# Kernel optimization log

Hardware: AMD Instinct MI355X
Metric: run time of the kernel (lower is better)

## Reference

```python
import jax, jax.numpy as jnp
import numpy as np

N_NODES = 50000
N_EDGES = 800000
NFEAT = 64
HID = 64
NCLASS = 10


def setup_inputs() -> dict:
    key = jax.random.key(0)
    ks = jax.random.split(key, 12)
    x = jax.random.normal(ks[0], (N_NODES, NFEAT), dtype=jnp.float32)
    edge_index = jax.random.randint(ks[1], (2, N_EDGES), 0, N_NODES, dtype=jnp.int64)
    edge_attr = jax.random.uniform(ks[2], (N_EDGES,), dtype=jnp.float32)
    # GCNConv layer params (glorot-ish scale)
    W1 = jax.random.normal(ks[3], (NFEAT, HID), dtype=jnp.float32) / np.sqrt(NFEAT)
    b1 = jnp.zeros((HID,), dtype=jnp.float32)
    W2 = jax.random.normal(ks[4], (HID, HID), dtype=jnp.float32) / np.sqrt(HID)
    b2 = jnp.zeros((HID,), dtype=jnp.float32)
    fc1_w = jax.random.normal(ks[5], (HID, 128), dtype=jnp.float32) / np.sqrt(HID)
    fc1_b = jnp.zeros((128,), dtype=jnp.float32)
    fc2_w = jax.random.normal(ks[6], (128, NCLASS), dtype=jnp.float32) / np.sqrt(128.0)
    fc2_b = jnp.zeros((NCLASS,), dtype=jnp.float32)
    return {"x": x, "edge_index": edge_index, "edge_attr": edge_attr,
            "W1": W1, "b1": b1, "W2": W2, "b2": b2,
            "fc1_w": fc1_w, "fc1_b": fc1_b, "fc2_w": fc2_w, "fc2_b": fc2_b}


def reference(x, edge_index, edge_attr, W1, b1, W2, b2, fc1_w, fc1_b, fc2_w, fc2_b):
    N = x.shape[0]
    # add_self_loops: append (i, i) edges; self-loop edge weight = 1
    loops = jnp.arange(N, dtype=edge_index.dtype)
    row = jnp.concatenate([edge_index[0], loops])
    col = jnp.concatenate([edge_index[1], loops])
    ew = jnp.concatenate([edge_attr, jnp.ones((N,), dtype=x.dtype)])
    # symmetric degree normalization: deg = degree(row); D^{-1/2} A D^{-1/2}
    deg = jax.ops.segment_sum(jnp.ones_like(ew), row, num_segments=N)
    dis = deg ** -0.5  # deg >= 1 due to self loops
    norm_w = dis[row] * ew * dis[col]  # [E+N]

    def gcn_conv(h, W, b):
        h = h @ W                                    # [N, d_out]
        msg = norm_w[:, None] * h[col]               # [E+N, d_out] gather
        agg = jax.ops.segment_sum(msg, row, num_segments=N)  # scatter-add
        return agg + b

    h = jax.nn.relu(gcn_conv(x, W1, b1))  # dropout is identity in eval mode
    h = gcn_conv(h, W2, b2)               # no activation after last conv
    h = jax.nn.relu(h @ fc1_w + fc1_b)
    return h @ fc2_w + fc2_b
```

## Files before the change

kernel.cpp:

```cpp
#include <hip/hip_runtime.h>


#define NFEAT 64


__global__ void k_hist(const int* __restrict__ row, int* __restrict__ cnt, int ne) {
    int i = blockIdx.x * blockDim.x + threadIdx.x;
    int st = gridDim.x * blockDim.x;
    for (; i < ne; i += st) atomicAdd(&cnt[row[i]], 1);
}

__global__ void k_scanA(const int* __restrict__ cnt, int* __restrict__ bsum, int n) {
    __shared__ int s[256];
    int tid = threadIdx.x;
    int i = blockIdx.x * 256 + tid;
    s[tid] = (i < n) ? cnt[i] : 0;
    __syncthreads();
    for (int d = 128; d > 0; d >>= 1) {
        if (tid < d) s[tid] += s[tid + d];
        __syncthreads();
    }
    if (tid == 0) bsum[blockIdx.x] = s[0];
}

__global__ void k_scanB(const int* __restrict__ bsum, int* __restrict__ bpre, int nb) {
    __shared__ int s[256];
    int tid = threadIdx.x;
    int v = (tid < nb) ? bsum[tid] : 0;
    s[tid] = v;
    __syncthreads();
    for (int d = 1; d < 256; d <<= 1) {
        int t = (tid >= d) ? s[tid - d] : 0;
        __syncthreads();
        s[tid] += t;
        __syncthreads();
    }
    if (tid < nb) bpre[tid] = s[tid] - v;
}

__global__ void k_scanC(const int* __restrict__ cnt, const int* __restrict__ bpre,
                        int* __restrict__ off, float* __restrict__ dis, int n) {
    __shared__ int s[256];
    int tid = threadIdx.x;
    int i = blockIdx.x * 256 + tid;
    int v = (i < n) ? cnt[i] : 0;
    s[tid] = v;
    __syncthreads();
    for (int d = 1; d < 256; d <<= 1) {
        int t = (tid >= d) ? s[tid - d] : 0;
        __syncthreads();
        s[tid] += t;
        __syncthreads();
    }
    if (i < n) {
        off[i] = bpre[blockIdx.x] + s[tid] - v;
        dis[i] = rsqrtf(1.0f + (float)v);
    }
}

__global__ void k_fill(const int* __restrict__ row, const int* __restrict__ col,
                       const float* __restrict__ ew, const float* __restrict__ dis,
                       int* __restrict__ off, int2* __restrict__ csr, int ne) {
    int i = blockIdx.x * blockDim.x + threadIdx.x;
    if (i >= ne) return;
    int r = row[i], c = col[i];
    float w = dis[r] * ew[i] * dis[c];
    int slot = atomicAdd(&off[r], 1);
    csr[slot] = make_int2(c, __float_as_int(w));
}


__global__ __launch_bounds__(256) void k_gemm64(const float* __restrict__ X,
                                                const float* __restrict__ W,
                                                float* __restrict__ Y, int nrows) {
    __shared__ float Wl[64 * 64];
    __shared__ float XT[64 * 68];
    int tid = threadIdx.x;
    int r0 = blockIdx.x * 64;
    for (int i = tid; i < 64 * 64; i += 256) Wl[i] = W[i];
    for (int i = tid; i < 64 * 64; i += 256) {
        int r = i >> 6, k = i & 63;
        int rr = r0 + r;
        XT[k * 68 + r] = (rr < nrows) ? X[(size_t)r0 * 64 + i] : 0.f;
    }
    __syncthreads();
    int f4 = (tid & 15) * 4;
    int r4 = (tid >> 4) * 4;
    float acc[4][4];
#pragma unroll
    for (int i = 0; i < 4; ++i)
#pragma unroll
        for (int j = 0; j < 4; ++j) acc[i][j] = 0.f;
#pragma unroll 8
    for (int k = 0; k < 64; ++k) {
        float4 w = *(const float4*)&Wl[k * 64 + f4];
        float4 xv = *(const float4*)&XT[k * 68 + r4];
        float xs[4] = {xv.x, xv.y, xv.z, xv.w};
        float ws[4] = {w.x, w.y, w.z, w.w};
#pragma unroll
        for (int i = 0; i < 4; ++i)
#pragma unroll
            for (int j = 0; j < 4; ++j) acc[i][j] = fmaf(xs[i], ws[j], acc[i][j]);
    }
#pragma unroll
    for (int i = 0; i < 4; ++i) {
        int rr = r0 + r4 + i;
        if (rr < nrows) {
            float4 o = make_float4(acc[i][0], acc[i][1], acc[i][2], acc[i][3]);
            *(float4*)&Y[(size_t)rr * 64 + f4] = o;
        }
    }
}


__device__ __forceinline__ float4 agg_row(const int* off_end, const int* cnt,
                                          const int2* csr, const float* H,
                                          int node, int sub, int q4) {
    int endv = off_end[node];
    int s = endv - cnt[node];
    float4 acc = make_float4(0.f, 0.f, 0.f, 0.f);
    int e = s + sub;
    for (; e + 4 < endv; e += 8) {
        int2 p0 = csr[e];
        int2 p1 = csr[e + 4];
        float w0 = __int_as_float(p0.y);
        float w1 = __int_as_float(p1.y);
        float4 h0 = *(const float4*)&H[(size_t)p0.x * 64 + q4];
        float4 h1 = *(const float4*)&H[(size_t)p1.x * 64 + q4];
        acc.x = fmaf(w0, h0.x, acc.x);
        acc.y = fmaf(w0, h0.y, acc.y);
        acc.z = fmaf(w0, h0.z, acc.z);
        acc.w = fmaf(w0, h0.w, acc.w);
        acc.x = fmaf(w1, h1.x, acc.x);
        acc.y = fmaf(w1, h1.y, acc.y);
        acc.z = fmaf(w1, h1.z, acc.z);
        acc.w = fmaf(w1, h1.w, acc.w);
    }
    if (e < endv) {
        int2 p = csr[e];
        float w = __int_as_float(p.y);
        float4 h = *(const float4*)&H[(size_t)p.x * 64 + q4];
        acc.x = fmaf(w, h.x, acc.x);
        acc.y = fmaf(w, h.y, acc.y);
        acc.z = fmaf(w, h.z, acc.z);
        acc.w = fmaf(w, h.w, acc.w);
    }
#pragma unroll
    for (int m = 16; m <= 32; m <<= 1) {
        acc.x += __shfl_xor(acc.x, m, 64);
        acc.y += __shfl_xor(acc.y, m, 64);
        acc.z += __shfl_xor(acc.z, m, 64);
        acc.w += __shfl_xor(acc.w, m, 64);
    }
    return acc;
}


__global__ __launch_bounds__(256) void k_agg(const int* __restrict__ off_end,
                                             const int* __restrict__ cnt,
                                             const float* __restrict__ dis,
                                             const int2* __restrict__ csr,
                                             const float* __restrict__ H,
                                             float* __restrict__ AGG, int n) {
    int l = threadIdx.x & 63;
    int node = (blockIdx.x * blockDim.x + threadIdx.x) >> 6;
    if (node >= n) return;
    int sub = l >> 4;
    int q4 = (l & 15) * 4;
    float4 acc = agg_row(off_end, cnt, csr, H, node, sub, q4);
    if (sub == 0) {
        float d = dis[node];
        float d2 = d * d;
        float4 hs = *(const float4*)&H[(size_t)node * 64 + q4];
        acc.x = fmaf(d2, hs.x, acc.x);
        acc.y = fmaf(d2, hs.y, acc.y);
        acc.z = fmaf(d2, hs.z, acc.z);
        acc.w = fmaf(d2, hs.w, acc.w);
        *(float4*)&AGG[(size_t)node * 64 + q4] = acc;
    }
}


__global__ __launch_bounds__(256) void k_agg_fused(const int* __restrict__ off_end,
                                                   const int* __restrict__ cnt,
                                                   const float* __restrict__ dis,
                                                   const int2* __restrict__ csr,
                                                   const float* __restrict__ H1,
                                                   const float* __restrict__ b1,
                                                   const float* __restrict__ W2,
                                                   float* __restrict__ H2, int n) {
    __shared__ float W2l[64 * 64];
    __shared__ float pbuf[4][64];
    int tid = threadIdx.x;
    for (int i = tid; i < 64 * 64; i += 256) W2l[i] = W2[i];
    __syncthreads();
    int l = tid & 63;
    int wv = tid >> 6;
    int sub = l >> 4;
    int q4 = (l & 15) * 4;
    int nwaves = (gridDim.x * blockDim.x) >> 6;
    for (int node = (blockIdx.x * blockDim.x + tid) >> 6; node < n; node += nwaves) {
        float4 acc = agg_row(off_end, cnt, csr, H1, node, sub, q4);
        float d = dis[node];
        float d2 = d * d;
        float4 hs = *(const float4*)&H1[(size_t)node * 64 + q4];
        float4 bq = *(const float4*)&b1[q4];
        float4 p;
        p.x = fmaxf(fmaf(d2, hs.x, acc.x) + bq.x, 0.f);
        p.y = fmaxf(fmaf(d2, hs.y, acc.y) + bq.y, 0.f);
        p.z = fmaxf(fmaf(d2, hs.z, acc.z) + bq.z, 0.f);
        p.w = fmaxf(fmaf(d2, hs.w, acc.w) + bq.w, 0.f);
        if (sub == 0) *(float4*)&pbuf[wv][q4] = p;
        asm volatile("s_waitcnt lgkmcnt(0)" ::: "memory");
        float sum = 0.f;
#pragma unroll
        for (int q = 0; q < 16; ++q) {
            float4 v = *(const float4*)&pbuf[wv][q * 4];
            sum = fmaf(v.x, W2l[(q * 4 + 0) * 64 + l], sum);
            sum = fmaf(v.y, W2l[(q * 4 + 1) * 64 + l], sum);
            sum = fmaf(v.z, W2l[(q * 4 + 2) * 64 + l], sum);
            sum = fmaf(v.w, W2l[(q * 4 + 3) * 64 + l], sum);
        }
        asm volatile("s_waitcnt lgkmcnt(0)" ::: "memory");
        H2[(size_t)node * 64 + l] = sum;
    }
}


__global__ __launch_bounds__(256, 4) void k_mlp(const float* __restrict__ AGG,
                                                const float* __restrict__ b2,
                                                const float* __restrict__ fc1w,
                                                const float* __restrict__ fc1b,
                                                const float* __restrict__ fc2w,
                                                const float* __restrict__ fc2b,
                                                float* __restrict__ out, int n) {
    __shared__ float XT[64 * 68];
    __shared__ float Wh[64 * 64];
    __shared__ float W2l[128 * 10];
    __shared__ float b1l[128];
    __shared__ float b2c[16];
    int tid = threadIdx.x;
    int r0 = blockIdx.x * 64;
    for (int i = tid; i < 64 * 64; i += 256) {
        int r = i >> 6, k = i & 63;
        int rr = r0 + r;
        float v = 0.f;
        if (rr < n) v = AGG[(size_t)r0 * 64 + i] + b2[k];
        XT[k * 68 + r] = v;
    }
    for (int i = tid; i < 64 * 64; i += 256)
        Wh[i] = fc1w[(i >> 6) * 128 + (i & 63)];
    for (int i = tid; i < 128 * 10; i += 256) W2l[i] = fc2w[i];
    if (tid < 128) b1l[tid] = fc1b[tid];
    if (tid < 10) b2c[tid] = fc2b[tid];
    __syncthreads();

    int f4 = (tid & 15) * 4;
    int r4 = (tid >> 4) * 4;
    float pacc[4][10];
#pragma unroll
    for (int i = 0; i < 4; ++i)
#pragma unroll
        for (int c = 0; c < 10; ++c) pacc[i][c] = 0.f;

#pragma unroll
    for (int h = 0; h < 2; ++h) {
        if (h == 1) {
            __syncthreads();
            for (int i = tid; i < 64 * 64; i += 256)
                Wh[i] = fc1w[(i >> 6) * 128 + 64 + (i & 63)];
            __syncthreads();
        }
        float acc[4][4];
#pragma unroll
        for (int i = 0; i < 4; ++i)
#pragma unroll
            for (int j = 0; j < 4; ++j) acc[i][j] = 0.f;
#pragma unroll 8
        for (int k = 0; k < 64; ++k) {
            float4 xv = *(const float4*)&XT[k * 68 + r4];
            float4 wv = *(const float4*)&Wh[k * 64 + f4];
            float xs[4] = {xv.x, xv.y, xv.z, xv.w};
            float ws[4] = {wv.x, wv.y, wv.z, wv.w};
#pragma unroll
            for (int i = 0; i < 4; ++i)
#pragma unroll
                for (int j = 0; j < 4; ++j) acc[i][j] = fmaf(xs[i], ws[j], acc[i][j]);
        }
#pragma unroll
        for (int jj = 0; jj < 4; ++jj) {
            int jcol = h * 64 + f4 + jj;
            float w2r[10];
#pragma unroll
            for (int c = 0; c < 10; ++c) w2r[c] = W2l[jcol * 10 + c];
            float bj = b1l[jcol];
#pragma unroll
            for (int i = 0; i < 4; ++i) {
                float pv = fmaxf(acc[i][jj] + bj, 0.f);
#pragma unroll
                for (int c = 0; c < 10; ++c) pacc[i][c] = fmaf(pv, w2r[c], pacc[i][c]);
            }
        }
    }
#pragma unroll
    for (int i = 0; i < 4; ++i)
#pragma unroll
        for (int c = 0; c < 10; ++c) {
            float v = pacc[i][c];
            v += __shfl_xor(v, 1, 64);
            v += __shfl_xor(v, 2, 64);
            v += __shfl_xor(v, 4, 64);
            v += __shfl_xor(v, 8, 64);
            pacc[i][c] = v;
        }
    if ((tid & 15) == 0) {
#pragma unroll
        for (int i = 0; i < 4; ++i) {
            int rr = r0 + r4 + i;
            if (rr < n) {
#pragma unroll
                for (int c = 0; c < 10; ++c)
                    out[(size_t)rr * 10 + c] = pacc[i][c] + b2c[c];
            }
        }
    }
}


extern "C" void kernel_launch(void* const* d_in, const int* in_sizes, int n_in,
                              void* d_out, int out_size, void* d_ws, size_t ws_size,
                              hipStream_t stream) {
    const float* x     = (const float*)d_in[0];
    const int*   eidx  = (const int*)d_in[1];
    const float* eattr = (const float*)d_in[2];
    const float* W1    = (const float*)d_in[3];
    const float* b1    = (const float*)d_in[4];
    const float* W2    = (const float*)d_in[5];
    const float* b2    = (const float*)d_in[6];
    const float* fc1w  = (const float*)d_in[7];
    const float* fc1b  = (const float*)d_in[8];
    const float* fc2w  = (const float*)d_in[9];
    const float* fc2b  = (const float*)d_in[10];
    float* out = (float*)d_out;

    const int N = in_sizes[0] / NFEAT;
    const int E = in_sizes[2];
    const int* row = eidx;
    const int* col = eidx + E;

    int*   icnt = (int*)d_ws;
    int*   off  = icnt + 50176;
    float* dis  = (float*)(off + 50176);
    int*   bsum = (int*)(dis + 50176);
    int*   bpre = bsum + 256;
    int2*  csr  = (int2*)(bpre + 256);
    float* H    = (float*)(csr + E);
    float* AGG  = H + (size_t)N * 64;

    const int TB = 256;
    int gN = (N + TB - 1) / TB;
    int gG = (N + 63) / 64;
    int gA = (N * 64 + TB - 1) / TB;
    int gE1 = (E + TB - 1) / TB;
    int nb = gN;

    hipMemsetAsync(icnt, 0, (size_t)N * sizeof(int), stream);
    k_hist<<<1024, TB, 0, stream>>>(row, icnt, E);
    k_scanA<<<nb, TB, 0, stream>>>(icnt, bsum, N);
    k_scanB<<<1, TB, 0, stream>>>(bsum, bpre, nb);
    k_scanC<<<nb, TB, 0, stream>>>(icnt, bpre, off, dis, N);
    k_fill<<<gE1, TB, 0, stream>>>(row, col, eattr, dis, off, csr, E);

    k_gemm64<<<gG, TB, 0, stream>>>(x, W1, H, N);
    k_agg_fused<<<2048, TB, 0, stream>>>(off, icnt, dis, csr, H, b1, W2, AGG, N);
    k_agg<<<gA, TB, 0, stream>>>(off, icnt, dis, csr, AGG, H, N);
    k_mlp<<<gG, TB, 0, stream>>>(H, b2, fc1w, fc1b, fc2w, fc2b, out, N);
}
```

Baseline: 284.4 us.

## Fuse second-layer aggregation into the MLP kernel via shared-memory tile

Removes the standalone second aggregation kernel and has each MLP block aggregate its own 64 nodes (one wave per 16 nodes) straight into the transposed shared tile, adding the bias on the fly. This avoids writing and re-reading the N×64 aggregated intermediate from global memory and drops one kernel launch. In exchange, the MLP kernel now carries the latency-bound gather work, and each block has only 4 waves processing nodes serially, which may lower memory-level parallelism compared with the old one-wave-per-node grid.

```diff
diff --git a/kernel.cpp b/kernel.cpp
--- a/kernel.cpp
+++ b/kernel.cpp
@@ -156,31 +156,6 @@
 }
 
 
-__global__ __launch_bounds__(256) void k_agg(const int* __restrict__ off_end,
-                                             const int* __restrict__ cnt,
-                                             const float* __restrict__ dis,
-                                             const int2* __restrict__ csr,
-                                             const float* __restrict__ H,
-                                             float* __restrict__ AGG, int n) {
-    int l = threadIdx.x & 63;
-    int node = (blockIdx.x * blockDim.x + threadIdx.x) >> 6;
-    if (node >= n) return;
-    int sub = l >> 4;
-    int q4 = (l & 15) * 4;
-    float4 acc = agg_row(off_end, cnt, csr, H, node, sub, q4);
-    if (sub == 0) {
-        float d = dis[node];
-        float d2 = d * d;
-        float4 hs = *(const float4*)&H[(size_t)node * 64 + q4];
-        acc.x = fmaf(d2, hs.x, acc.x);
-        acc.y = fmaf(d2, hs.y, acc.y);
-        acc.z = fmaf(d2, hs.z, acc.z);
-        acc.w = fmaf(d2, hs.w, acc.w);
-        *(float4*)&AGG[(size_t)node * 64 + q4] = acc;
-    }
-}
-
-
 __global__ __launch_bounds__(256) void k_agg_fused(const int* __restrict__ off_end,
                                                    const int* __restrict__ cnt,
                                                    const float* __restrict__ dis,
@@ -227,32 +202,57 @@
 }
 
 
-__global__ __launch_bounds__(256, 4) void k_mlp(const float* __restrict__ AGG,
-                                                const float* __restrict__ b2,
-                                                const float* __restrict__ fc1w,
-                                                const float* __restrict__ fc1b,
-                                                const float* __restrict__ fc2w,
-                                                const float* __restrict__ fc2b,
-                                                float* __restrict__ out, int n) {
+__global__ __launch_bounds__(256, 4) void k_agg_mlp(const int* __restrict__ off_end,
+                                                    const int* __restrict__ cnt,
+                                                    const float* __restrict__ dis,
+                                                    const int2* __restrict__ csr,
+                                                    const float* __restrict__ H2,
+                                                    const float* __restrict__ b2,
+                                                    const float* __restrict__ fc1w,
+                                                    const float* __restrict__ fc1b,
+                                                    const float* __restrict__ fc2w,
+                                                    const float* __restrict__ fc2b,
+                                                    float* __restrict__ out, int n) {
     __shared__ float XT[64 * 68];
     __shared__ float Wh[64 * 64];
     __shared__ float W2l[128 * 10];
     __shared__ float b1l[128];
     __shared__ float b2c[16];
+    __shared__ float b2in[64];
     int tid = threadIdx.x;
     int r0 = blockIdx.x * 64;
-    for (int i = tid; i < 64 * 64; i += 256) {
-        int r = i >> 6, k = i & 63;
-        int rr = r0 + r;
-        float v = 0.f;
-        if (rr < n) v = AGG[(size_t)r0 * 64 + i] + b2[k];
-        XT[k * 68 + r] = v;
-    }
     for (int i = tid; i < 64 * 64; i += 256)
         Wh[i] = fc1w[(i >> 6) * 128 + (i & 63)];
     for (int i = tid; i < 128 * 10; i += 256) W2l[i] = fc2w[i];
     if (tid < 128) b1l[tid] = fc1b[tid];
     if (tid < 10) b2c[tid] = fc2b[tid];
+    if (tid < 64) b2in[tid] = b2[tid];
+
+    int l = tid & 63;
+    int wv = tid >> 6;
+    int sub = l >> 4;
+    int q4 = (l & 15) * 4;
+    for (int t = 0; t < 16; ++t) {
+        int r = wv * 16 + t;
+        int node = r0 + r;
+        if (node < n) {
+            float4 acc = agg_row(off_end, cnt, csr, H2, node, sub, q4);
+            if (sub == 0) {
+                float d = dis[node];
+                float d2 = d * d;
+                float4 hs = *(const float4*)&H2[(size_t)node * 64 + q4];
+                XT[(q4 + 0) * 68 + r] = fmaf(d2, hs.x, acc.x) + b2in[q4 + 0];
+                XT[(q4 + 1) * 68 + r] = fmaf(d2, hs.y, acc.y) + b2in[q4 + 1];
+                XT[(q4 + 2) * 68 + r] = fmaf(d2, hs.z, acc.z) + b2in[q4 + 2];
+                XT[(q4 + 3) * 68 + r] = fmaf(d2, hs.w, acc.w) + b2in[q4 + 3];
+            }
+        } else if (sub == 0) {
+            XT[(q4 + 0) * 68 + r] = 0.f;
+            XT[(q4 + 1) * 68 + r] = 0.f;
+            XT[(q4 + 2) * 68 + r] = 0.f;
+            XT[(q4 + 3) * 68 + r] = 0.f;
+        }
+    }
     __syncthreads();
 
     int f4 = (tid & 15) * 4;
@@ -279,9 +279,9 @@
 #pragma unroll 8
         for (int k = 0; k < 64; ++k) {
             float4 xv = *(const float4*)&XT[k * 68 + r4];
-            float4 wv = *(const float4*)&Wh[k * 64 + f4];
+            float4 wv4 = *(const float4*)&Wh[k * 64 + f4];
             float xs[4] = {xv.x, xv.y, xv.z, xv.w};
-            float ws[4] = {wv.x, wv.y, wv.z, wv.w};
+            float ws[4] = {wv4.x, wv4.y, wv4.z, wv4.w};
 #pragma unroll
             for (int i = 0; i < 4; ++i)
 #pragma unroll
@@ -355,12 +355,11 @@
     int*   bpre = bsum + 256;
     int2*  csr  = (int2*)(bpre + 256);
     float* H    = (float*)(csr + E);
-    float* AGG  = H + (size_t)N * 64;
+    float* H2   = H + (size_t)N * 64;
 
     const int TB = 256;
     int gN = (N + TB - 1) / TB;
     int gG = (N + 63) / 64;
-    int gA = (N * 64 + TB - 1) / TB;
     int gE1 = (E + TB - 1) / TB;
     int nb = gN;
 
@@ -372,7 +371,7 @@
     k_fill<<<gE1, TB, 0, stream>>>(row, col, eattr, dis, off, csr, E);
 
     k_gemm64<<<gG, TB, 0, stream>>>(x, W1, H, N);
-    k_agg_fused<<<2048, TB, 0, stream>>>(off, icnt, dis, csr, H, b1, W2, AGG, N);
-    k_agg<<<gA, TB, 0, stream>>>(off, icnt, dis, csr, AGG, H, N);
-    k_mlp<<<gG, TB, 0, stream>>>(H, b2, fc1w, fc1b, fc2w, fc2b, out, N);
-}
+    k_agg_fused<<<2048, TB, 0, stream>>>(off, icnt, dis, csr, H, b1, W2, H2, N);
+    k_agg_mlp<<<gG, TB, 0, stream>>>(off, icnt, dis, csr, H2, b2,
+                                     fc1w, fc1b, fc2w, fc2b, out, N);
+}
```

After: 293.0 us. 1.03x slower.
